# Performance work log

Measured on AMD Instinct MI355X. Metric: run time of the kernel, lower is better.

## Reference

```python
import jax, jax.numpy as jnp
import numpy as np

NV, NE, H, P = 50000, 10000, 256, 400000

def setup_inputs() -> dict:
    key = jax.random.key(0)
    ks = jax.random.split(key, 16)
    s = 1.0 / np.sqrt(H)
    return {
        "v": jax.random.normal(ks[0], (NV, H), jnp.float32),
        "e": jax.random.normal(ks[1], (NE, H), jnp.float32),
        "W_v2e_w": jax.random.normal(ks[2], (H, H), jnp.float32) * s,
        "W_v2e_b": jnp.zeros((H,), jnp.float32),
        "W_e2v_w": jax.random.normal(ks[3], (H, H), jnp.float32) * s,
        "W_e2v_b": jnp.zeros((H,), jnp.float32),
        "n_weight": jax.random.uniform(ks[4], (NV, 1), jnp.float32),
        "e_weight": jax.random.uniform(ks[5], (NE, 1), jnp.float32),
        "n_reg_weight": jax.random.uniform(ks[6], (P, 1), jnp.float32),
        "e_reg_weight": jax.random.uniform(ks[7], (P, 1), jnp.float32),
        "e_reg_sum": jax.random.uniform(ks[8], (NE, 1), jnp.float32) + 1.0,  # positive normalizer
        "n_reg_sum": jax.random.uniform(ks[9], (NV, 1), jnp.float32) + 1.0,
        "pairs_v": jax.random.randint(ks[10], (P,), 0, NV, jnp.int32),  # ve_lists[:,0]
        "eidx": jax.random.randint(ks[11], (P,), 0, NE, jnp.int32),
        "pairs_e": jax.random.randint(ks[12], (P,), 0, NE, jnp.int32),  # ve_lists[:,1]
        "vidx": jax.random.randint(ks[13], (P,), 0, NV, jnp.int32),
    }

def reference(v, e, W_v2e_w, W_v2e_b, W_e2v_w, W_e2v_b, n_weight, e_weight,
              n_reg_weight, e_reg_weight, e_reg_sum, n_reg_sum,
              pairs_v, eidx, pairs_e, vidx):
    # v2e: dense transform on vertices, gather per incidence, scatter-add into edges
    ve = jax.nn.relu(v @ W_v2e_w.T + W_v2e_b)            # [NV,H]
    v_acc = v * n_weight                                 # v *= n_weight * v_fac(=1)
    msg_ve = (ve * n_weight)[pairs_v] * n_reg_weight     # [P,H]
    e_out = e.at[eidx].add(msg_ve) / e_reg_sum           # [NE,H]
    # e2v: dense transform on edges, gather per incidence, scatter-add into vertices
    ev = jax.nn.relu(e_out @ W_e2v_w.T + W_e2v_b)        # [NE,H]
    msg_ev = (ev * e_weight)[pairs_e] * e_reg_weight     # [P,H]
    v_out = v_acc.at[vidx].add(msg_ev) / n_reg_sum       # [NV,H]
    return v_out, e_out
```

## Files before the change

### kernel.cpp

```cpp
#include <hip/hip_runtime.h>
#include <stdint.h>

#define NV 50000
#define NE 10000
#define HD 256
#define NP 400000

#define SE 96
#define SV 40

#define NCH 64
#define CHP (NP / NCH)
#define NW  15000

#define PREP_HBLK NCH
#define PREP_WBLK 16
#define PREP_VBLK 1563

typedef short short8 __attribute__((ext_vector_type(8)));
typedef short short4v __attribute__((ext_vector_type(4)));
typedef float f32x4 __attribute__((ext_vector_type(4)));

__device__ __forceinline__ short f2bf(float f) {
    unsigned int u = __builtin_bit_cast(unsigned int, f);
    u += 0x7FFFu + ((u >> 16) & 1u);
    return (short)(u >> 16);
}
__device__ __forceinline__ float bf2f(short s) {
    unsigned int u = ((unsigned int)(unsigned short)s) << 16;
    return __builtin_bit_cast(float, u);
}

__global__ __launch_bounds__(1024) void prep_kernel(
    const float* __restrict__ v, const float* __restrict__ W1, const float* __restrict__ W2,
    const int* __restrict__ eidx, const int* __restrict__ vidx,
    short* __restrict__ v_bf, short* __restrict__ W_bf,
    int* __restrict__ cnt8,
    int conv_v)
{
    __shared__ int h[NW];
    int b = blockIdx.x;
    int tid = threadIdx.x;
    if (b < PREP_HBLK) {
        for (int w = tid; w < NW; w += 1024) h[w] = 0;
        __syncthreads();
        int base = b * CHP;
        for (int k = tid; k < CHP; k += 1024) {
            int p = base + k;
            int er = eidx[p];
            atomicAdd((unsigned*)&h[er >> 2], 1u << ((er & 3) * 8));
            int rv = 10000 + vidx[p];
            atomicAdd((unsigned*)&h[rv >> 2], 1u << ((rv & 3) * 8));
        }
        __syncthreads();
        for (int w = tid; w < NW; w += 1024) cnt8[b * NW + w] = h[w];
    } else if (b < PREP_HBLK + PREP_WBLK) {
        size_t i = (size_t)(b - PREP_HBLK) * 8192 + (size_t)tid * 8;
        const float* src = (i < 65536) ? (W1 + i) : (W2 + (i - 65536));
        float4 a0 = *(const float4*)src;
        float4 a1 = *(const float4*)(src + 4);
        short8 s;
        s[0] = f2bf(a0.x); s[1] = f2bf(a0.y); s[2] = f2bf(a0.z); s[3] = f2bf(a0.w);
        s[4] = f2bf(a1.x); s[5] = f2bf(a1.y); s[6] = f2bf(a1.z); s[7] = f2bf(a1.w);
        *(short8*)(W_bf + i) = s;
    } else {
        if (!conv_v) return;
        size_t i = (size_t)(b - PREP_HBLK - PREP_WBLK) * 8192 + (size_t)tid * 8;
        if (i >= (size_t)NV * HD) return;
        float4 a0 = *(const float4*)(v + i);
        float4 a1 = *(const float4*)(v + i + 4);
        short8 s;
        s[0] = f2bf(a0.x); s[1] = f2bf(a0.y); s[2] = f2bf(a0.z); s[3] = f2bf(a0.w);
        s[4] = f2bf(a1.x); s[5] = f2bf(a1.y); s[6] = f2bf(a1.z); s[7] = f2bf(a1.w);
        *(short8*)(v_bf + i) = s;
    }
}

__global__ __launch_bounds__(256) void scan_kernel(
    int* __restrict__ cnt8, int* __restrict__ cnt_e, int* __restrict__ cnt_v)
{
    int w = blockIdx.x * 256 + threadIdx.x;
    if (w >= NW) return;
    unsigned acc = 0;
#pragma unroll 4
    for (int c = 0; c < NCH; ++c) {
        unsigned x = (unsigned)cnt8[c * NW + w];
        cnt8[c * NW + w] = (int)acc;
        acc += x;
    }
    int r0 = w * 4;
    int4 t;
    t.x = acc & 0xFF; t.y = (acc >> 8) & 0xFF; t.z = (acc >> 16) & 0xFF; t.w = acc >> 24;
    if (r0 < 10000) *(int4*)&cnt_e[r0] = t;
    else            *(int4*)&cnt_v[r0 - 10000] = t;
}

__global__ __launch_bounds__(1024) void place_kernel(
    const int* __restrict__ eidx, const int* __restrict__ vidx,
    const int* __restrict__ pairs_v, const int* __restrict__ n_reg_w_bits,
    const int* __restrict__ pairs_e, const int* __restrict__ e_reg_w_bits,
    const int* __restrict__ cnt8,
    int2* __restrict__ bkt_e, int2* __restrict__ bkt_v)
{
    __shared__ int h[NW];
    int c = blockIdx.x;
    int tid = threadIdx.x;
    for (int w = tid; w < NW; w += 1024) h[w] = cnt8[c * NW + w];
    __syncthreads();
    int base = c * CHP;
    for (int k = tid; k < CHP; k += 1024) {
        int p = base + k;
        int er = eidx[p];
        unsigned old = atomicAdd((unsigned*)&h[er >> 2], 1u << ((er & 3) * 8));
        int s = (old >> ((er & 3) * 8)) & 0xFF;
        if (s < SE) bkt_e[er * SE + s] = make_int2(pairs_v[p], n_reg_w_bits[p]);
        int rv = 10000 + vidx[p];
        old = atomicAdd((unsigned*)&h[rv >> 2], 1u << ((rv & 3) * 8));
        s = (old >> ((rv & 3) * 8)) & 0xFF;
        if (s < SV) bkt_v[(rv - 10000) * SV + s] = make_int2(pairs_e[p], e_reg_w_bits[p]);
    }
}

__global__ __launch_bounds__(256) void gemm_rs(
    const void* __restrict__ Av, int a_bf,
    const short* __restrict__ Wb,
    const float* __restrict__ bias,
    const float* __restrict__ rowscale,
    short* __restrict__ out,
    int M)
{
    __shared__ short As[64 * 256];
    __shared__ short Ws[64 * 256];
    const int tid  = threadIdx.x;
    const int row0 = blockIdx.x * 64;

#pragma unroll
    for (int it = 0; it < 8; ++it) {
        int cl = it * 256 + tid;
        int r  = cl >> 5;
        int c  = cl & 31;
        int gr = row0 + r; gr = gr < M ? gr : M - 1;
        short8 ap;
        if (a_bf) {
            ap = *(const short8*)((const short*)Av + (size_t)gr * HD + (c << 3));
        } else {
            const float* asrc = (const float*)Av + (size_t)gr * HD + (c << 3);
            float4 a0 = *(const float4*)asrc;
            float4 a1 = *(const float4*)(asrc + 4);
            ap[0] = f2bf(a0.x); ap[1] = f2bf(a0.y); ap[2] = f2bf(a0.z); ap[3] = f2bf(a0.w);
            ap[4] = f2bf(a1.x); ap[5] = f2bf(a1.y); ap[6] = f2bf(a1.z); ap[7] = f2bf(a1.w);
        }
        *(short8*)&As[(r << 8) + ((c ^ (r & 7)) << 3)] = ap;
    }

    const int lane = tid & 63;
    const int wv   = tid >> 6;
    const int m16  = lane & 15;
    const int quad = lane >> 4;
    const int arow = (wv << 4) + m16;

    for (int ct = 0; ct < 4; ++ct) {
        __syncthreads();
#pragma unroll
        for (int it = 0; it < 8; ++it) {
            int cl = it * 256 + tid;
            int r  = cl >> 5;
            int c  = cl & 31;
            short8 wp = *(const short8*)(Wb + (size_t)((ct << 6) + r) * HD + (c << 3));
            *(short8*)&Ws[(r << 8) + ((c ^ (r & 7)) << 3)] = wp;
        }
        __syncthreads();

        f32x4 acc[4];
#pragma unroll
        for (int nt = 0; nt < 4; ++nt) acc[nt] = (f32x4){0.f, 0.f, 0.f, 0.f};

#pragma unroll
        for (int ks = 0; ks < 8; ++ks) {
            int c = (ks << 2) + quad;
            short8 afr = *(const short8*)&As[(arow << 8) + ((c ^ (arow & 7)) << 3)];
#pragma unroll
            for (int nt = 0; nt < 4; ++nt) {
                int brow = (nt << 4) + m16;
                short8 bfr = *(const short8*)&Ws[(brow << 8) + ((c ^ (m16 & 7)) << 3)];
                acc[nt] = __builtin_amdgcn_mfma_f32_16x16x32_bf16(afr, bfr, acc[nt], 0, 0, 0);
            }
        }

#pragma unroll
        for (int r = 0; r < 4; ++r) {
            int row = row0 + (wv << 4) + (quad << 2) + r;
            if (row < M) {
                float rs = rowscale[row];
#pragma unroll
                for (int nt = 0; nt < 4; ++nt) {
                    int col = (ct << 6) + (nt << 4) + m16;
                    float val = acc[nt][r] + bias[col];
                    val = fmaxf(val, 0.0f) * rs;
                    out[(size_t)row * HD + col] = f2bf(val);
                }
            }
        }
    }
}

__device__ __forceinline__ void gather_core(
    const short* __restrict__ msg, const int2* __restrict__ bkt,
    int i, int end, int lane, float4& acc)
{
    while (i < end) {
        int n = end - i; n = n < 64 ? n : 64;
        int src = 0; float w = 0.f;
        if (lane < n) {
            int2 m = bkt[i + lane];
            src = m.x;
            w = __builtin_bit_cast(float, m.y);
        }
        int j = 0;
        for (; j + 4 <= n; j += 4) {
            int   s0 = __shfl(src, j),     s1 = __shfl(src, j + 1);
            int   s2 = __shfl(src, j + 2), s3 = __shfl(src, j + 3);
            float w0 = __shfl(w, j),       w1 = __shfl(w, j + 1);
            float w2 = __shfl(w, j + 2),   w3 = __shfl(w, j + 3);
            short4v m0 = *(const short4v*)(msg + ((size_t)s0 << 8) + (lane << 2));
            short4v m1 = *(const short4v*)(msg + ((size_t)s1 << 8) + (lane << 2));
            short4v m2 = *(const short4v*)(msg + ((size_t)s2 << 8) + (lane << 2));
            short4v m3 = *(const short4v*)(msg + ((size_t)s3 << 8) + (lane << 2));
            acc.x += bf2f(m0[0]) * w0; acc.y += bf2f(m0[1]) * w0;
            acc.z += bf2f(m0[2]) * w0; acc.w += bf2f(m0[3]) * w0;
            acc.x += bf2f(m1[0]) * w1; acc.y += bf2f(m1[1]) * w1;
            acc.z += bf2f(m1[2]) * w1; acc.w += bf2f(m1[3]) * w1;
            acc.x += bf2f(m2[0]) * w2; acc.y += bf2f(m2[1]) * w2;
            acc.z += bf2f(m2[2]) * w2; acc.w += bf2f(m2[3]) * w2;
            acc.x += bf2f(m3[0]) * w3; acc.y += bf2f(m3[1]) * w3;
            acc.z += bf2f(m3[2]) * w3; acc.w += bf2f(m3[3]) * w3;
        }
        for (; j < n; ++j) {
            int s0 = __shfl(src, j); float w0 = __shfl(w, j);
            short4v m0 = *(const short4v*)(msg + ((size_t)s0 << 8) + (lane << 2));
            acc.x += bf2f(m0[0]) * w0; acc.y += bf2f(m0[1]) * w0;
            acc.z += bf2f(m0[2]) * w0; acc.w += bf2f(m0[3]) * w0;
        }
        i += n;
    }
}

__global__ __launch_bounds__(256) void gather_e(
    const short* __restrict__ msg,
    const int2* __restrict__ bkt,
    const int* __restrict__ cnt,
    const float* __restrict__ e_in, const float* __restrict__ reg_sum,
    float* __restrict__ out, short* __restrict__ out_bf)
{
    int r    = (blockIdx.x << 2) + (threadIdx.x >> 6);
    int lane = threadIdx.x & 63;
    float4 acc = ((const float4*)(e_in + (size_t)r * HD))[lane];
    int n = cnt[r]; n = n < SE ? n : SE;
    int i0 = r * SE;
    gather_core(msg, bkt, i0, i0 + n, lane, acc);
    float inv = 1.0f / reg_sum[r];
    acc.x *= inv; acc.y *= inv; acc.z *= inv; acc.w *= inv;
    ((float4*)(out + (size_t)r * HD))[lane] = acc;
    if (out_bf) {
        short4v s;
        s[0] = f2bf(acc.x); s[1] = f2bf(acc.y); s[2] = f2bf(acc.z); s[3] = f2bf(acc.w);
        *(short4v*)(out_bf + (size_t)r * HD + (lane << 2)) = s;
    }
}

__global__ __launch_bounds__(256) void gather_v(
    const short* __restrict__ msg,
    const int2* __restrict__ bkt,
    const int* __restrict__ cnt,
    const float* __restrict__ v_f32, const short* __restrict__ v_bf,
    const float* __restrict__ n_w,
    const float* __restrict__ reg_sum, float* __restrict__ out)
{
    int r    = (blockIdx.x << 2) + (threadIdx.x >> 6);
    int lane = threadIdx.x & 63;
    float nw = n_w[r];
    float4 a;
    if (v_bf) {
        short4v b = *(const short4v*)(v_bf + (size_t)r * HD + (lane << 2));
        a.x = bf2f(b[0]); a.y = bf2f(b[1]); a.z = bf2f(b[2]); a.w = bf2f(b[3]);
    } else {
        a = ((const float4*)(v_f32 + (size_t)r * HD))[lane];
    }
    float4 acc; acc.x = a.x * nw; acc.y = a.y * nw; acc.z = a.z * nw; acc.w = a.w * nw;
    int n = cnt[r]; n = n < SV ? n : SV;
    int i0 = r * SV;
    gather_core(msg, bkt, i0, i0 + n, lane, acc);
    float inv = 1.0f / reg_sum[r];
    acc.x *= inv; acc.y *= inv; acc.z *= inv; acc.w *= inv;
    ((float4*)(out + (size_t)r * HD))[lane] = acc;
}

extern "C" void kernel_launch(void* const* d_in, const int* in_sizes, int n_in,
                              void* d_out, int out_size, void* d_ws, size_t ws_size,
                              hipStream_t stream) {
    const float* v   = (const float*)d_in[0];
    const float* e   = (const float*)d_in[1];
    const float* W1  = (const float*)d_in[2];
    const float* b1  = (const float*)d_in[3];
    const float* W2  = (const float*)d_in[4];
    const float* b2  = (const float*)d_in[5];
    const float* n_weight     = (const float*)d_in[6];
    const float* e_weight     = (const float*)d_in[7];
    const float* n_reg_weight = (const float*)d_in[8];
    const float* e_reg_weight = (const float*)d_in[9];
    const float* e_reg_sum    = (const float*)d_in[10];
    const float* n_reg_sum    = (const float*)d_in[11];
    const int* pairs_v = (const int*)d_in[12];
    const int* eidx    = (const int*)d_in[13];
    const int* pairs_e = (const int*)d_in[14];
    const int* vidx    = (const int*)d_in[15];

    float* out      = (float*)d_out;
    float* v_region = out;
    float* e_region = out + (size_t)NV * HD;

    char* ws = (char*)d_ws;
    size_t o = 0;
    short* msg     = (short*)(ws + o); o += (size_t)NV * HD * 2;
    int2*  bkt_e   = (int2*)(ws + o);  o += (size_t)NE * SE * 8;
    int2*  bkt_v   = (int2*)(ws + o);  o += (size_t)NV * SV * 8;
    short* W_bf    = (short*)(ws + o); o += (size_t)2 * 65536 * 2;
    int*   cnt8    = (int*)(ws + o);
    short* e_bf    = (short*)(ws + o); o += (size_t)NE * HD * 2;
    int*   cnt_e   = (int*)(ws + o);   o += (size_t)NE * 4;
    int*   cnt_v   = (int*)(ws + o);   o += (size_t)NV * 4;
    size_t o_opt = o;
    short* v_bf    = (short*)(ws + o_opt);
    size_t need_full = o_opt + (size_t)NV * HD * 2;
    const int full = (ws_size >= need_full);

    prep_kernel<<<PREP_HBLK + PREP_WBLK + PREP_VBLK, 1024, 0, stream>>>(
        v, W1, W2, eidx, vidx, full ? v_bf : (short*)msg , W_bf,
        cnt8, full);
    scan_kernel<<<(NW + 255) / 256, 256, 0, stream>>>(cnt8, cnt_e, cnt_v);
    place_kernel<<<NCH, 1024, 0, stream>>>(
        eidx, vidx, pairs_v, (const int*)n_reg_weight,
        pairs_e, (const int*)e_reg_weight, cnt8, bkt_e, bkt_v);

    gemm_rs<<<(NV + 63) / 64, 256, 0, stream>>>(
        full ? (const void*)v_bf : (const void*)v, full, W_bf, b1, n_weight, msg, NV);
    gather_e<<<NE / 4, 256, 0, stream>>>(msg, bkt_e, cnt_e,
        e, e_reg_sum, e_region, e_bf);
    gemm_rs<<<(NE + 63) / 64, 256, 0, stream>>>(
        (const void*)e_bf, 1, W_bf + 65536, b2, e_weight, msg, NE);
    gather_v<<<NV / 4, 256, 0, stream>>>(msg, bkt_v, cnt_v,
        v, full ? v_bf : (short*)0, n_weight, n_reg_sum, v_region);
}
```

Measured before the change: 299.8 us.

## Split placement into separate edge and vertex blocks with more chunks

The bucket placement kernel now launches separate block sets for edge and vertex incidences. The incidence list is also cut into twice as many chunks, so four times as many blocks run and each loads a smaller slice of the packed counter histogram into shared memory. Bucket capacities SE and SV are reduced, which shrinks the bucket arrays the gather kernels read but raises the chance that overflow entries get silently dropped. The per-chunk counter array doubles in size and now shares workspace space with e_bf, and the prefix-scan loop has to walk more chunks.

```diff
diff --git a/kernel.cpp b/kernel.cpp
--- a/kernel.cpp
+++ b/kernel.cpp
@@ -6,12 +6,14 @@
 #define HD 256
 #define NP 400000
 
-#define SE 96
-#define SV 40
-
-#define NCH 64
+#define SE 88
+#define SV 36
+
+#define NCH 128
 #define CHP (NP / NCH)
 #define NW  15000
+#define NWE 2500
+#define NWV 12500
 
 #define PREP_HBLK NCH
 #define PREP_WBLK 16
@@ -82,7 +84,7 @@
     int w = blockIdx.x * 256 + threadIdx.x;
     if (w >= NW) return;
     unsigned acc = 0;
-#pragma unroll 4
+#pragma unroll 8
     for (int c = 0; c < NCH; ++c) {
         unsigned x = (unsigned)cnt8[c * NW + w];
         cnt8[c * NW + w] = (int)acc;
@@ -102,22 +104,33 @@
     const int* __restrict__ cnt8,
     int2* __restrict__ bkt_e, int2* __restrict__ bkt_v)
 {
-    __shared__ int h[NW];
-    int c = blockIdx.x;
+    __shared__ int h[NWV];
+    int b = blockIdx.x;
     int tid = threadIdx.x;
-    for (int w = tid; w < NW; w += 1024) h[w] = cnt8[c * NW + w];
-    __syncthreads();
-    int base = c * CHP;
-    for (int k = tid; k < CHP; k += 1024) {
-        int p = base + k;
-        int er = eidx[p];
-        unsigned old = atomicAdd((unsigned*)&h[er >> 2], 1u << ((er & 3) * 8));
-        int s = (old >> ((er & 3) * 8)) & 0xFF;
-        if (s < SE) bkt_e[er * SE + s] = make_int2(pairs_v[p], n_reg_w_bits[p]);
-        int rv = 10000 + vidx[p];
-        old = atomicAdd((unsigned*)&h[rv >> 2], 1u << ((rv & 3) * 8));
-        s = (old >> ((rv & 3) * 8)) & 0xFF;
-        if (s < SV) bkt_v[(rv - 10000) * SV + s] = make_int2(pairs_e[p], e_reg_w_bits[p]);
+    if (b < NCH) {
+        int c = b;
+        for (int w = tid; w < NWE; w += 1024) h[w] = cnt8[c * NW + w];
+        __syncthreads();
+        int base = c * CHP;
+        for (int k = tid; k < CHP; k += 1024) {
+            int p = base + k;
+            int er = eidx[p];
+            unsigned old = atomicAdd((unsigned*)&h[er >> 2], 1u << ((er & 3) * 8));
+            int s = (old >> ((er & 3) * 8)) & 0xFF;
+            if (s < SE) bkt_e[er * SE + s] = make_int2(pairs_v[p], n_reg_w_bits[p]);
+        }
+    } else {
+        int c = b - NCH;
+        for (int w = tid; w < NWV; w += 1024) h[w] = cnt8[c * NW + NWE + w];
+        __syncthreads();
+        int base = c * CHP;
+        for (int k = tid; k < CHP; k += 1024) {
+            int p = base + k;
+            int vr = vidx[p];
+            unsigned old = atomicAdd((unsigned*)&h[vr >> 2], 1u << ((vr & 3) * 8));
+            int s = (old >> ((vr & 3) * 8)) & 0xFF;
+            if (s < SV) bkt_v[vr * SV + s] = make_int2(pairs_e[p], e_reg_w_bits[p]);
+        }
     }
 }
 
@@ -326,7 +339,7 @@
     int2*  bkt_v   = (int2*)(ws + o);  o += (size_t)NV * SV * 8;
     short* W_bf    = (short*)(ws + o); o += (size_t)2 * 65536 * 2;
     int*   cnt8    = (int*)(ws + o);
-    short* e_bf    = (short*)(ws + o); o += (size_t)NE * HD * 2;
+    short* e_bf    = (short*)(ws + o); o += (size_t)NCH * NW * 4;
     int*   cnt_e   = (int*)(ws + o);   o += (size_t)NE * 4;
     int*   cnt_v   = (int*)(ws + o);   o += (size_t)NV * 4;
     size_t o_opt = o;
@@ -338,7 +351,7 @@
         v, W1, W2, eidx, vidx, full ? v_bf : (short*)msg , W_bf,
         cnt8, full);
     scan_kernel<<<(NW + 255) / 256, 256, 0, stream>>>(cnt8, cnt_e, cnt_v);
-    place_kernel<<<NCH, 1024, 0, stream>>>(
+    place_kernel<<<2 * NCH, 1024, 0, stream>>>(
         eidx, vidx, pairs_v, (const int*)n_reg_weight,
         pairs_e, (const int*)e_reg_weight, cnt8, bkt_e, bkt_v);
 
```

Result: faster. 275.1 us (-8.2%).
